# Optimization experiments

Hardware: AMD Instinct MI355X
Metric: run time of the kernel (lower is better)

The kernel has to match this reference:

```python
import jax, jax.numpy as jnp
import numpy as np

BUF_SLOTS = 524288
N_LOC = 32768
NOPE_DIM = 512
ROPE_DIM = 64


def setup_inputs() -> dict:
    key = jax.random.key(0)
    k1, k2 = jax.random.split(key)
    kv_buffer = jnp.zeros((BUF_SLOTS, NOPE_DIM + ROPE_DIM), dtype=jnp.float32)
    loc = jnp.arange(N_LOC, dtype=jnp.int32)  # unique slot indices into kv_buffer
    cache_k_nope = jax.random.normal(k1, (N_LOC, NOPE_DIM), dtype=jnp.float32)
    cache_k_rope = jax.random.normal(k2, (N_LOC, ROPE_DIM), dtype=jnp.float32)
    return {"kv_buffer": kv_buffer, "loc": loc,
            "cache_k_nope": cache_k_nope, "cache_k_rope": cache_k_rope}


def reference(kv_buffer, loc, cache_k_nope, cache_k_rope):
    # Concatenate nope+rope per token, then scatter rows into the paged buffer.
    kv = jnp.concatenate([cache_k_nope, cache_k_rope], axis=-1)  # [n_loc, total_dim]
    return kv_buffer.at[loc].set(kv, unique_indices=True)
```

## Files before the change

### kernel.cpp

```cpp
#include <hip/hip_runtime.h>
#include <hip/hip_bf16.h>


#define BUF_SLOTS 524288
#define N_LOC     32768
#define ROW_F     576
#define ROW_V     144
#define NOPE_V    128
#define ROPE_V    16

__global__ __launch_bounds__(256) void scatter_rows(
    const int* __restrict__ loc,
    const float4* __restrict__ nope,
    const float4* __restrict__ rope,
    float4* __restrict__ out)
{
    const int tid = blockIdx.x * blockDim.x + threadIdx.x;
    const int n_nope = N_LOC * NOPE_V;
    if (tid < n_nope) {
        const int token = tid >> 7;
        const int j     = tid & (NOPE_V - 1);
        const int row   = loc[token];
        out[(size_t)row * ROW_V + j] = nope[(size_t)token * NOPE_V + j];
    } else {
        const int t2    = tid - n_nope;
        const int token = t2 >> 4;
        const int j     = t2 & (ROPE_V - 1);
        const int row   = loc[token];
        out[(size_t)row * ROW_V + NOPE_V + j] = rope[(size_t)token * ROPE_V + j];
    }
}

extern "C" void kernel_launch(void* const* d_in, const int* in_sizes, int n_in,
                              void* d_out, int out_size, void* d_ws, size_t ws_size,
                              hipStream_t stream)
{
    const float*  kv_buffer = (const float*)d_in[0];
    const int*    loc       = (const int*)d_in[1];
    const float4* nope      = (const float4*)d_in[2];
    const float4* rope      = (const float4*)d_in[3];
    float*        out       = (float*)d_out;

    const size_t buf_bytes = (size_t)BUF_SLOTS * ROW_F * sizeof(float);
    hipMemcpyAsync(out, kv_buffer, buf_bytes, hipMemcpyDeviceToDevice, stream);

    const int total_threads = N_LOC * (NOPE_V + ROPE_V);
    const int block = 256;
    const int grid  = total_threads / block;
    scatter_rows<<<grid, block, 0, stream>>>(loc, nope, rope, (float4*)out);
}
```

Measured before the change: 2.050 ms.

## Fuse buffer copy and scatter via inverse slot map in workspace

Builds an inverse map from buffer slot to token index in the workspace, then writes every output element in a single pass, taking it either from the original buffer or from the new nope/rope rows. This avoids copying the full buffer and then rewriting the scattered rows, so those rows are no longer read from the old buffer and written twice. It adds two small kernels to initialise and fill the map, plus a per-element map lookup. When the workspace is too small it falls back to a custom copy kernel followed by the original scatter.

```diff
diff --git a/kernel.cpp b/kernel.cpp
--- a/kernel.cpp
+++ b/kernel.cpp
@@ -4,10 +4,50 @@
 
 #define BUF_SLOTS 524288
 #define N_LOC     32768
-#define ROW_F     576
 #define ROW_V     144
 #define NOPE_V    128
 #define ROPE_V    16
+
+__global__ __launch_bounds__(256) void init_mark(int* __restrict__ mark)
+{
+    const int tid = blockIdx.x * 256 + threadIdx.x;
+    if (tid < BUF_SLOTS) mark[tid] = -1;
+}
+
+__global__ __launch_bounds__(256) void build_mark(const int* __restrict__ loc,
+                                                  int* __restrict__ mark)
+{
+    const int tid = blockIdx.x * 256 + threadIdx.x;
+    if (tid < N_LOC) mark[loc[tid]] = tid;
+}
+
+__global__ __launch_bounds__(256) void fused_write(
+    const float4* __restrict__ kv,
+    const float4* __restrict__ nope,
+    const float4* __restrict__ rope,
+    const int*    __restrict__ mark,
+    float4*       __restrict__ out)
+{
+    const int t   = blockIdx.x * 256 + threadIdx.x;
+    const int row = t / ROW_V;
+    const int j   = t - row * ROW_V;
+    const int m   = mark[row];
+    float4 v;
+    if (m < 0) {
+        v = kv[t];
+    } else {
+        v = (j < NOPE_V) ? nope[m * NOPE_V + j]
+                         : rope[m * ROPE_V + (j - NOPE_V)];
+    }
+    out[t] = v;
+}
+
+__global__ __launch_bounds__(256) void copy_buf(const float4* __restrict__ src,
+                                                float4* __restrict__ dst)
+{
+    const int t = blockIdx.x * 256 + threadIdx.x;
+    dst[t] = src[t];
+}
 
 __global__ __launch_bounds__(256) void scatter_rows(
     const int* __restrict__ loc,
@@ -15,7 +55,7 @@
     const float4* __restrict__ rope,
     float4* __restrict__ out)
 {
-    const int tid = blockIdx.x * blockDim.x + threadIdx.x;
+    const int tid = blockIdx.x * 256 + threadIdx.x;
     const int n_nope = N_LOC * NOPE_V;
     if (tid < n_nope) {
         const int token = tid >> 7;
@@ -35,17 +75,22 @@
                               void* d_out, int out_size, void* d_ws, size_t ws_size,
                               hipStream_t stream)
 {
-    const float*  kv_buffer = (const float*)d_in[0];
-    const int*    loc       = (const int*)d_in[1];
-    const float4* nope      = (const float4*)d_in[2];
-    const float4* rope      = (const float4*)d_in[3];
-    float*        out       = (float*)d_out;
+    const float4* kv   = (const float4*)d_in[0];
+    const int*    loc  = (const int*)d_in[1];
+    const float4* nope = (const float4*)d_in[2];
+    const float4* rope = (const float4*)d_in[3];
+    float4*       out  = (float4*)d_out;
 
-    const size_t buf_bytes = (size_t)BUF_SLOTS * ROW_F * sizeof(float);
-    hipMemcpyAsync(out, kv_buffer, buf_bytes, hipMemcpyDeviceToDevice, stream);
-
-    const int total_threads = N_LOC * (NOPE_V + ROPE_V);
-    const int block = 256;
-    const int grid  = total_threads / block;
-    scatter_rows<<<grid, block, 0, stream>>>(loc, nope, rope, (float4*)out);
+    if (ws_size >= (size_t)BUF_SLOTS * sizeof(int)) {
+        int* mark = (int*)d_ws;
+        init_mark<<<BUF_SLOTS / 256, 256, 0, stream>>>(mark);
+        build_mark<<<N_LOC / 256, 256, 0, stream>>>(loc, mark);
+        const int total = BUF_SLOTS * ROW_V;
+        fused_write<<<total / 256, 256, 0, stream>>>(kv, nope, rope, mark, out);
+    } else {
+        const int total = BUF_SLOTS * ROW_V;
+        copy_buf<<<total / 256, 256, 0, stream>>>(kv, out);
+        const int sthreads = N_LOC * (NOPE_V + ROPE_V);
+        scatter_rows<<<sthreads / 256, 256, 0, stream>>>(loc, nope, rope, out);
+    }
 }
```

Measured after the change: 1.839 ms. 1.11x faster.
